# Kernel optimization log

Hardware: AMD Instinct MI355X
Metric: run time of the kernel (lower is better)

## Reference

```python
import jax, jax.numpy as jnp
import numpy as np

# Static config (matches init_kwargs)
THR = 0.2
BORDER = 2
TEMP = 0.1
H0C, W0C = 60, 80
H1C, W1C = 60, 80
HW0_I = (480, 640)
SCALE = HW0_I[0] / H0C  # = 8.0, coarse->image scale


def setup_inputs() -> dict:
    key = jax.random.key(0)
    k0, k1 = jax.random.split(key)
    feat0 = jax.random.normal(k0, (4, H0C * W0C, 256), dtype=jnp.float32)
    feat1 = jax.random.normal(k1, (4, H1C * W1C, 256), dtype=jnp.float32)
    return {"feat0": feat0, "feat1": feat1}


def _valid_axis(n):
    i = jnp.arange(n)
    return (i >= BORDER) & (i < n - BORDER)


def reference(feat0, feat1):
    B, L, C = feat0.shape
    S = feat1.shape[1]
    inv_sqrt_c = 1.0 / jnp.sqrt(jnp.asarray(C, feat0.dtype))
    f0 = feat0 * inv_sqrt_c
    f1 = feat1 * inv_sqrt_c
    # similarity + dual softmax -> confidence matrix [B, L, S]
    sim = jnp.einsum("blc,bsc->bls", f0, f1) / TEMP
    conf = jax.nn.softmax(sim, axis=1) * jax.nn.softmax(sim, axis=2)

    # threshold + border removal (static border, no padding masks)
    mask = conf > THR
    m5 = mask.reshape(B, H0C, W0C, H1C, W1C)
    m5 = (m5
          & _valid_axis(H0C)[None, :, None, None, None]
          & _valid_axis(W0C)[None, None, :, None, None]
          & _valid_axis(H1C)[None, None, None, :, None]
          & _valid_axis(W1C)[None, None, None, None, :])
    mask = m5.reshape(B, L, S)

    # mutual nearest: keep conf only where it is both the row max and the col max
    score = mask.astype(conf.dtype) * jnp.max(conf, axis=2, keepdims=True) * jnp.max(conf, axis=1, keepdims=True)
    mask_max_values = jnp.max(score, axis=2)          # [B, L]
    s_ids = jnp.argmax(score, axis=2)                 # [B, L]
    match = mask_max_values > 0                       # [B, L] dense stand-in for torch.where
    mconf = jnp.take_along_axis(conf, s_ids[:, :, None], axis=2)[..., 0]
    mconf = jnp.where(match, mconf, jnp.zeros_like(mconf))

    # coarse keypoint coordinates
    l = jnp.arange(L)
    mkpts0 = jnp.stack([l % W0C, l // W0C], axis=1).astype(conf.dtype) * SCALE          # [L, 2]
    mkpts1 = jnp.stack([s_ids % W1C, s_ids // W1C], axis=-1).astype(conf.dtype) * SCALE  # [B, L, 2]
    return conf, match, s_ids, mconf, mkpts0, mkpts1
```

## Files before the change

### kernel.cpp

```cpp
#include <hip/hip_runtime.h>
#include <math.h>

#define B_ 4
#define L_ 4800
#define S_ 4800
#define C_ 256
#define THR 0.2f
#define SIM_SCALE 0.0390625f
#define KPT_SCALE 8.0f

typedef short bf16x8 __attribute__((ext_vector_type(8)));
typedef float f32x4  __attribute__((ext_vector_type(4)));


__device__ __forceinline__ unsigned short f2bf(float x) {
    union { float f; unsigned int u; } v; v.f = x;
    unsigned int r = v.u + 0x7fffu + ((v.u >> 16) & 1u);
    return (unsigned short)(r >> 16);
}

__global__ void k_init(float* ws) {
    int i = blockIdx.x * blockDim.x + threadIdx.x;
    if (i < 76800) ws[i] = 0.0f;
}

__global__ void k_cast(const float* __restrict__ f0, const float* __restrict__ f1,
                       ushort* __restrict__ f0b, ushort* __restrict__ f1b) {
    int i = blockIdx.x * blockDim.x + threadIdx.x;
    if (i * 4 >= B_ * L_ * C_) return;
    float4 a = ((const float4*)f0)[i];
    float4 b = ((const float4*)f1)[i];
    ushort4 oa, ob;
    oa.x = f2bf(a.x); oa.y = f2bf(a.y); oa.z = f2bf(a.z); oa.w = f2bf(a.w);
    ob.x = f2bf(b.x); ob.y = f2bf(b.y); ob.z = f2bf(b.z); ob.w = f2bf(b.w);
    ((ushort4*)f0b)[i] = oa;
    ((ushort4*)f1b)[i] = ob;
}

__global__ __launch_bounds__(256) void k_gemm(
        const ushort* __restrict__ f0b, const ushort* __restrict__ f1b,
        float* __restrict__ p_out,
        float* __restrict__ rowsum, float* __restrict__ colsum) {
    const int b    = blockIdx.z;
    const int l0   = blockIdx.y * 64;
    const int wave = threadIdx.x >> 6;
    const int s0   = blockIdx.x * 256 + wave * 64;
    if (s0 >= S_) return;
    const int lane = threadIdx.x & 63;
    const int quad = lane >> 4;
    const int lr   = lane & 15;

    const ushort* A  = f0b + (size_t)b * L_ * C_;
    const ushort* Bm = f1b + (size_t)b * S_ * C_;

    f32x4 acc[4][4];
#pragma unroll
    for (int r = 0; r < 4; r++)
#pragma unroll
        for (int c = 0; c < 4; c++) acc[r][c] = (f32x4){0.f, 0.f, 0.f, 0.f};

    for (int kk = 0; kk < C_; kk += 32) {
        bf16x8 af[4], bf[4];
#pragma unroll
        for (int r = 0; r < 4; r++) {
            const int row = l0 + r * 16 + lr;
            af[r] = *(const bf16x8*)(A + (size_t)row * C_ + kk + quad * 8);
        }
#pragma unroll
        for (int c = 0; c < 4; c++) {
            const int srow = s0 + c * 16 + lr;
            bf[c] = *(const bf16x8*)(Bm + (size_t)srow * C_ + kk + quad * 8);
        }
#pragma unroll
        for (int r = 0; r < 4; r++)
#pragma unroll
            for (int c = 0; c < 4; c++)
                acc[r][c] = __builtin_amdgcn_mfma_f32_16x16x32_bf16(af[r], bf[c], acc[r][c], 0, 0, 0);
    }

#pragma unroll
    for (int r = 0; r < 4; r++)
#pragma unroll
        for (int c = 0; c < 4; c++)
#pragma unroll
            for (int g = 0; g < 4; g++)
                acc[r][c][g] = __expf(acc[r][c][g] * SIM_SCALE);

    float* pb = p_out + (size_t)b * L_ * S_;
#pragma unroll
    for (int r = 0; r < 4; r++)
#pragma unroll
        for (int g = 0; g < 4; g++) {
            const int row = l0 + r * 16 + quad * 4 + g;
            float* prow = pb + (size_t)row * S_ + s0 + lr;
#pragma unroll
            for (int c = 0; c < 4; c++) prow[c * 16] = acc[r][c][g];
        }

#pragma unroll
    for (int r = 0; r < 4; r++)
#pragma unroll
        for (int g = 0; g < 4; g++) {
            float v = acc[r][0][g] + acc[r][1][g] + acc[r][2][g] + acc[r][3][g];
            v += __shfl_xor(v, 1, 64);
            v += __shfl_xor(v, 2, 64);
            v += __shfl_xor(v, 4, 64);
            v += __shfl_xor(v, 8, 64);
            if (lr == 0) {
                const int row = l0 + r * 16 + quad * 4 + g;
                atomicAdd(rowsum + b * L_ + row, v);
            }
        }
#pragma unroll
    for (int c = 0; c < 4; c++) {
        float v = 0.f;
#pragma unroll
        for (int r = 0; r < 4; r++)
#pragma unroll
            for (int g = 0; g < 4; g++) v += acc[r][c][g];
        v += __shfl_xor(v, 16, 64);
        v += __shfl_xor(v, 32, 64);
        if (quad == 0) atomicAdd(colsum + b * S_ + s0 + c * 16 + lr, v);
    }
}

__global__ __launch_bounds__(256) void k_conf(
        float* __restrict__ conf,
        const float* __restrict__ rowsum, const float* __restrict__ colsum,
        float* __restrict__ rowmax, float* __restrict__ colmax) {
    const int b  = blockIdx.z;
    const int l0 = blockIdx.y * 64;
    const int s0 = blockIdx.x * 64;
    __shared__ unsigned rm[64], cm[64];
    const int t = threadIdx.x;
    if (t < 64) { rm[t] = 0u; cm[t] = 0u; }
    __syncthreads();
    const int c4 = t & 15, r0 = t >> 4;
    const float4 cs = *(const float4*)(colsum + b * S_ + s0 + c4 * 4);
    const float icx = 1.0f / cs.x, icy = 1.0f / cs.y, icz = 1.0f / cs.z, icw = 1.0f / cs.w;
    float cmx = 0.f, cmy = 0.f, cmz = 0.f, cmw = 0.f;
    float* base = conf + (size_t)b * L_ * S_;
#pragma unroll
    for (int it = 0; it < 4; it++) {
        const int r = r0 + 16 * it;
        const int l = l0 + r;
        const float irs = 1.0f / rowsum[b * L_ + l];
        float* addr = base + (size_t)l * S_ + s0 + c4 * 4;
        float4 p = *(float4*)addr;
        float4 cf;
        cf.x = p.x * p.x * (irs * icx);
        cf.y = p.y * p.y * (irs * icy);
        cf.z = p.z * p.z * (irs * icz);
        cf.w = p.w * p.w * (irs * icw);
        *(float4*)addr = cf;
        const float m = fmaxf(fmaxf(cf.x, cf.y), fmaxf(cf.z, cf.w));
        atomicMax(&rm[r], __float_as_uint(m));
        cmx = fmaxf(cmx, cf.x); cmy = fmaxf(cmy, cf.y);
        cmz = fmaxf(cmz, cf.z); cmw = fmaxf(cmw, cf.w);
    }
    atomicMax(&cm[c4 * 4 + 0], __float_as_uint(cmx));
    atomicMax(&cm[c4 * 4 + 1], __float_as_uint(cmy));
    atomicMax(&cm[c4 * 4 + 2], __float_as_uint(cmz));
    atomicMax(&cm[c4 * 4 + 3], __float_as_uint(cmw));
    __syncthreads();
    if (t < 64) {
        atomicMax((unsigned*)rowmax + b * L_ + l0 + t, rm[t]);
        atomicMax((unsigned*)colmax + b * S_ + s0 + t, cm[t]);
    }
}

__global__ __launch_bounds__(256) void k_match(
        const float* __restrict__ conf,
        const float* __restrict__ rowmax, const float* __restrict__ colmax,
        float* __restrict__ o_match, float* __restrict__ o_sids,
        float* __restrict__ o_mconf, float* __restrict__ o_kp0,
        float* __restrict__ o_kp1) {
    const int l = blockIdx.x;
    const int b = blockIdx.y;
    const int t = threadIdx.x;
    const int lh = l / 80, lw = l % 80;
    const bool lvalid = (lh >= 2 && lh < 58 && lw >= 2 && lw < 78);

    __shared__ float sv[256];
    __shared__ int   si[256];

    float bv = 0.0f; int bi = 0;
    if (lvalid) {
        const float* row = conf + ((size_t)b * L_ + l) * S_;
        const float  rmv = rowmax[b * L_ + l];
        const float* cmr = colmax + b * S_;
        for (int i = t; i < S_ / 4; i += 256) {
            const float4 cf = *(const float4*)(row + i * 4);
            float cv; int s;
#define PROC(comp, off)                                                        \
            cv = cf.comp; s = i * 4 + off;                                     \
            if (cv > THR) {                                                    \
                const int sh = s / 80, sw = s % 80;                            \
                if (sh >= 2 && sh < 58 && sw >= 2 && sw < 78) {                \
                    const float sc = rmv * cmr[s];                             \
                    if (sc > bv || (sc == bv && s < bi)) { bv = sc; bi = s; }  \
                }                                                              \
            }
            PROC(x, 0) PROC(y, 1) PROC(z, 2) PROC(w, 3)
#undef PROC
        }
    }
    sv[t] = bv; si[t] = bi;
    __syncthreads();
    for (int off = 128; off > 0; off >>= 1) {
        if (t < off) {
            const float v2 = sv[t + off]; const int i2 = si[t + off];
            if (v2 > sv[t] || (v2 == sv[t] && i2 < si[t])) { sv[t] = v2; si[t] = i2; }
        }
        __syncthreads();
    }
    if (t == 0) {
        const float maxv = sv[0]; const int sid = si[0];
        const bool match = maxv > 0.0f;
        float mc = 0.0f;
        if (match) mc = conf[((size_t)b * L_ + l) * S_ + sid];
        const int o = b * L_ + l;
        o_match[o] = match ? 1.0f : 0.0f;
        o_sids[o]  = (float)sid;
        o_mconf[o] = mc;
        o_kp1[o * 2 + 0] = (float)(sid % 80) * KPT_SCALE;
        o_kp1[o * 2 + 1] = (float)(sid / 80) * KPT_SCALE;
        if (b == 0) {
            o_kp0[l * 2 + 0] = (float)lw * KPT_SCALE;
            o_kp0[l * 2 + 1] = (float)lh * KPT_SCALE;
        }
    }
}

extern "C" void kernel_launch(void* const* d_in, const int* in_sizes, int n_in,
                              void* d_out, int out_size, void* d_ws, size_t ws_size,
                              hipStream_t stream) {
    const float* f0 = (const float*)d_in[0];
    const float* f1 = (const float*)d_in[1];
    float* out = (float*)d_out;

    float* conf_o  = out;
    float* o_match = out + (size_t)92160000;
    float* o_sids  = o_match + 19200;
    float* o_mconf = o_sids + 19200;
    float* o_kp0   = o_mconf + 19200;
    float* o_kp1   = o_kp0 + 9600;

    float* wsf    = (float*)d_ws;
    float* rowsum = wsf;
    float* colsum = wsf + 19200;
    float* rowmax = wsf + 38400;
    float* colmax = wsf + 57600;
    ushort* f0b = (ushort*)(wsf + 76800);
    ushort* f1b = f0b + (size_t)B_ * L_ * C_;

    k_init<<<300, 256, 0, stream>>>(wsf);
    k_cast<<<4800, 256, 0, stream>>>(f0, f1, f0b, f1b);
    k_gemm<<<dim3(19, 75, B_), 256, 0, stream>>>(f0b, f1b, conf_o, rowsum, colsum);
    k_conf<<<dim3(75, 75, B_), 256, 0, stream>>>(conf_o, rowsum, colsum, rowmax, colmax);
    k_match<<<dim3(L_, B_), 256, 0, stream>>>(conf_o, rowmax, colmax,
                                              o_match, o_sids, o_mconf, o_kp0, o_kp1);
}
```

Baseline: 754.7 us.

## Recompute GEMM in second pass to fuse normalization, maxima and sparse candidate extraction

Splits the similarity GEMM into two passes: the first only accumulates row/column sums of exp(sim), the second recomputes the tile, normalizes into conf, writes it once, updates row/col maxima, and appends above-threshold valid entries to a global candidate list. Separate scoring and emit kernels then resolve the per-row argmax via 64-bit atomicMax over candidates, replacing full-matrix read/rewrite and row-scan passes. This trades a second GEMM's compute for eliminating several passes over the large conf matrix, at the risk of overflowing the fixed candidate capacity.

Result: slower. 789.0 us (+4.5%).

```diff
diff --git a/kernel.cpp b/kernel.cpp
--- a/kernel.cpp
+++ b/kernel.cpp
@@ -8,10 +8,15 @@
 #define THR 0.2f
 #define SIM_SCALE 0.0390625f
 #define KPT_SCALE 8.0f
+#define CAND_CAP 262144u
 
 typedef short bf16x8 __attribute__((ext_vector_type(8)));
 typedef float f32x4  __attribute__((ext_vector_type(4)));
 
+#define WS_ZERO_N 115204
+#define WS_CAND_CNT 115200
+#define WS_CAND_LIST 115208
+#define WS_BF16 (115208 + CAND_CAP)
 
 __device__ __forceinline__ unsigned short f2bf(float x) {
     union { float f; unsigned int u; } v; v.f = x;
@@ -21,7 +26,7 @@
 
 __global__ void k_init(float* ws) {
     int i = blockIdx.x * blockDim.x + threadIdx.x;
-    if (i < 76800) ws[i] = 0.0f;
+    if (i < WS_ZERO_N) ws[i] = 0.0f;
 }
 
 __global__ void k_cast(const float* __restrict__ f0, const float* __restrict__ f1,
@@ -37,10 +42,13 @@
     ((ushort4*)f1b)[i] = ob;
 }
 
+template <int PASS>
 __global__ __launch_bounds__(256) void k_gemm(
         const ushort* __restrict__ f0b, const ushort* __restrict__ f1b,
-        float* __restrict__ p_out,
-        float* __restrict__ rowsum, float* __restrict__ colsum) {
+        float* __restrict__ conf,
+        float* __restrict__ rowsum, float* __restrict__ colsum,
+        float* __restrict__ rowmax, float* __restrict__ colmax,
+        unsigned* __restrict__ cand_cnt, unsigned* __restrict__ cand_list) {
     const int b    = blockIdx.z;
     const int l0   = blockIdx.y * 64;
     const int wave = threadIdx.x >> 6;
@@ -86,149 +94,161 @@
             for (int g = 0; g < 4; g++)
                 acc[r][c][g] = __expf(acc[r][c][g] * SIM_SCALE);
 
-    float* pb = p_out + (size_t)b * L_ * S_;
-#pragma unroll
-    for (int r = 0; r < 4; r++)
-#pragma unroll
-        for (int g = 0; g < 4; g++) {
-            const int row = l0 + r * 16 + quad * 4 + g;
-            float* prow = pb + (size_t)row * S_ + s0 + lr;
-#pragma unroll
-            for (int c = 0; c < 4; c++) prow[c * 16] = acc[r][c][g];
-        }
-
-#pragma unroll
-    for (int r = 0; r < 4; r++)
-#pragma unroll
-        for (int g = 0; g < 4; g++) {
-            float v = acc[r][0][g] + acc[r][1][g] + acc[r][2][g] + acc[r][3][g];
-            v += __shfl_xor(v, 1, 64);
-            v += __shfl_xor(v, 2, 64);
-            v += __shfl_xor(v, 4, 64);
-            v += __shfl_xor(v, 8, 64);
-            if (lr == 0) {
+    if constexpr (PASS == 0) {
+#pragma unroll
+        for (int r = 0; r < 4; r++)
+#pragma unroll
+            for (int g = 0; g < 4; g++) {
+                float v = acc[r][0][g] + acc[r][1][g] + acc[r][2][g] + acc[r][3][g];
+                v += __shfl_xor(v, 1, 64);
+                v += __shfl_xor(v, 2, 64);
+                v += __shfl_xor(v, 4, 64);
+                v += __shfl_xor(v, 8, 64);
+                if (lr == 0) {
+                    const int row = l0 + r * 16 + quad * 4 + g;
+                    atomicAdd(rowsum + b * L_ + row, v);
+                }
+            }
+#pragma unroll
+        for (int c = 0; c < 4; c++) {
+            float v = 0.f;
+#pragma unroll
+            for (int r = 0; r < 4; r++)
+#pragma unroll
+                for (int g = 0; g < 4; g++) v += acc[r][c][g];
+            v += __shfl_xor(v, 16, 64);
+            v += __shfl_xor(v, 32, 64);
+            if (quad == 0) atomicAdd(colsum + b * S_ + s0 + c * 16 + lr, v);
+        }
+    } else {
+        float irs[4][4];
+#pragma unroll
+        for (int r = 0; r < 4; r++)
+#pragma unroll
+            for (int g = 0; g < 4; g++)
+                irs[r][g] = 1.0f / rowsum[b * L_ + l0 + r * 16 + quad * 4 + g];
+        float ics[4];
+#pragma unroll
+        for (int c = 0; c < 4; c++)
+            ics[c] = 1.0f / colsum[b * S_ + s0 + c * 16 + lr];
+#pragma unroll
+        for (int r = 0; r < 4; r++)
+#pragma unroll
+            for (int c = 0; c < 4; c++)
+#pragma unroll
+                for (int g = 0; g < 4; g++) {
+                    const float p = acc[r][c][g];
+                    acc[r][c][g] = p * p * (irs[r][g] * ics[c]);
+                }
+
+        float* pb = conf + (size_t)b * L_ * S_;
+#pragma unroll
+        for (int r = 0; r < 4; r++)
+#pragma unroll
+            for (int g = 0; g < 4; g++) {
                 const int row = l0 + r * 16 + quad * 4 + g;
-                atomicAdd(rowsum + b * L_ + row, v);
+                float* prow = pb + (size_t)row * S_ + s0 + lr;
+#pragma unroll
+                for (int c = 0; c < 4; c++) prow[c * 16] = acc[r][c][g];
             }
-        }
-#pragma unroll
-    for (int c = 0; c < 4; c++) {
-        float v = 0.f;
-#pragma unroll
-        for (int r = 0; r < 4; r++)
-#pragma unroll
-            for (int g = 0; g < 4; g++) v += acc[r][c][g];
-        v += __shfl_xor(v, 16, 64);
-        v += __shfl_xor(v, 32, 64);
-        if (quad == 0) atomicAdd(colsum + b * S_ + s0 + c * 16 + lr, v);
-    }
-}
-
-__global__ __launch_bounds__(256) void k_conf(
-        float* __restrict__ conf,
-        const float* __restrict__ rowsum, const float* __restrict__ colsum,
-        float* __restrict__ rowmax, float* __restrict__ colmax) {
-    const int b  = blockIdx.z;
-    const int l0 = blockIdx.y * 64;
-    const int s0 = blockIdx.x * 64;
-    __shared__ unsigned rm[64], cm[64];
-    const int t = threadIdx.x;
-    if (t < 64) { rm[t] = 0u; cm[t] = 0u; }
-    __syncthreads();
-    const int c4 = t & 15, r0 = t >> 4;
-    const float4 cs = *(const float4*)(colsum + b * S_ + s0 + c4 * 4);
-    const float icx = 1.0f / cs.x, icy = 1.0f / cs.y, icz = 1.0f / cs.z, icw = 1.0f / cs.w;
-    float cmx = 0.f, cmy = 0.f, cmz = 0.f, cmw = 0.f;
-    float* base = conf + (size_t)b * L_ * S_;
-#pragma unroll
-    for (int it = 0; it < 4; it++) {
-        const int r = r0 + 16 * it;
-        const int l = l0 + r;
-        const float irs = 1.0f / rowsum[b * L_ + l];
-        float* addr = base + (size_t)l * S_ + s0 + c4 * 4;
-        float4 p = *(float4*)addr;
-        float4 cf;
-        cf.x = p.x * p.x * (irs * icx);
-        cf.y = p.y * p.y * (irs * icy);
-        cf.z = p.z * p.z * (irs * icz);
-        cf.w = p.w * p.w * (irs * icw);
-        *(float4*)addr = cf;
-        const float m = fmaxf(fmaxf(cf.x, cf.y), fmaxf(cf.z, cf.w));
-        atomicMax(&rm[r], __float_as_uint(m));
-        cmx = fmaxf(cmx, cf.x); cmy = fmaxf(cmy, cf.y);
-        cmz = fmaxf(cmz, cf.z); cmw = fmaxf(cmw, cf.w);
-    }
-    atomicMax(&cm[c4 * 4 + 0], __float_as_uint(cmx));
-    atomicMax(&cm[c4 * 4 + 1], __float_as_uint(cmy));
-    atomicMax(&cm[c4 * 4 + 2], __float_as_uint(cmz));
-    atomicMax(&cm[c4 * 4 + 3], __float_as_uint(cmw));
-    __syncthreads();
-    if (t < 64) {
-        atomicMax((unsigned*)rowmax + b * L_ + l0 + t, rm[t]);
-        atomicMax((unsigned*)colmax + b * S_ + s0 + t, cm[t]);
-    }
-}
-
-__global__ __launch_bounds__(256) void k_match(
-        const float* __restrict__ conf,
-        const float* __restrict__ rowmax, const float* __restrict__ colmax,
-        float* __restrict__ o_match, float* __restrict__ o_sids,
-        float* __restrict__ o_mconf, float* __restrict__ o_kp0,
-        float* __restrict__ o_kp1) {
-    const int l = blockIdx.x;
-    const int b = blockIdx.y;
-    const int t = threadIdx.x;
-    const int lh = l / 80, lw = l % 80;
-    const bool lvalid = (lh >= 2 && lh < 58 && lw >= 2 && lw < 78);
-
-    __shared__ float sv[256];
-    __shared__ int   si[256];
-
-    float bv = 0.0f; int bi = 0;
-    if (lvalid) {
-        const float* row = conf + ((size_t)b * L_ + l) * S_;
-        const float  rmv = rowmax[b * L_ + l];
-        const float* cmr = colmax + b * S_;
-        for (int i = t; i < S_ / 4; i += 256) {
-            const float4 cf = *(const float4*)(row + i * 4);
-            float cv; int s;
-#define PROC(comp, off)                                                        \
-            cv = cf.comp; s = i * 4 + off;                                     \
-            if (cv > THR) {                                                    \
-                const int sh = s / 80, sw = s % 80;                            \
-                if (sh >= 2 && sh < 58 && sw >= 2 && sw < 78) {                \
-                    const float sc = rmv * cmr[s];                             \
-                    if (sc > bv || (sc == bv && s < bi)) { bv = sc; bi = s; }  \
-                }                                                              \
+
+        float lane_max = 0.f;
+#pragma unroll
+        for (int r = 0; r < 4; r++)
+#pragma unroll
+            for (int g = 0; g < 4; g++) {
+                float m = fmaxf(fmaxf(acc[r][0][g], acc[r][1][g]),
+                                fmaxf(acc[r][2][g], acc[r][3][g]));
+                lane_max = fmaxf(lane_max, m);
+                m = fmaxf(m, __shfl_xor(m, 1, 64));
+                m = fmaxf(m, __shfl_xor(m, 2, 64));
+                m = fmaxf(m, __shfl_xor(m, 4, 64));
+                m = fmaxf(m, __shfl_xor(m, 8, 64));
+                if (lr == 0) {
+                    const int row = l0 + r * 16 + quad * 4 + g;
+                    atomicMax((unsigned*)rowmax + b * L_ + row, __float_as_uint(m));
+                }
             }
-            PROC(x, 0) PROC(y, 1) PROC(z, 2) PROC(w, 3)
-#undef PROC
-        }
-    }
-    sv[t] = bv; si[t] = bi;
-    __syncthreads();
-    for (int off = 128; off > 0; off >>= 1) {
-        if (t < off) {
-            const float v2 = sv[t + off]; const int i2 = si[t + off];
-            if (v2 > sv[t] || (v2 == sv[t] && i2 < si[t])) { sv[t] = v2; si[t] = i2; }
-        }
-        __syncthreads();
-    }
-    if (t == 0) {
-        const float maxv = sv[0]; const int sid = si[0];
-        const bool match = maxv > 0.0f;
-        float mc = 0.0f;
-        if (match) mc = conf[((size_t)b * L_ + l) * S_ + sid];
-        const int o = b * L_ + l;
-        o_match[o] = match ? 1.0f : 0.0f;
-        o_sids[o]  = (float)sid;
-        o_mconf[o] = mc;
-        o_kp1[o * 2 + 0] = (float)(sid % 80) * KPT_SCALE;
-        o_kp1[o * 2 + 1] = (float)(sid / 80) * KPT_SCALE;
-        if (b == 0) {
-            o_kp0[l * 2 + 0] = (float)lw * KPT_SCALE;
-            o_kp0[l * 2 + 1] = (float)lh * KPT_SCALE;
-        }
+#pragma unroll
+        for (int c = 0; c < 4; c++) {
+            float v = 0.f;
+#pragma unroll
+            for (int r = 0; r < 4; r++)
+#pragma unroll
+                for (int g = 0; g < 4; g++) v = fmaxf(v, acc[r][c][g]);
+            v = fmaxf(v, __shfl_xor(v, 16, 64));
+            v = fmaxf(v, __shfl_xor(v, 32, 64));
+            if (quad == 0)
+                atomicMax((unsigned*)colmax + b * S_ + s0 + c * 16 + lr, __float_as_uint(v));
+        }
+
+        if (__any(lane_max > THR)) {
+#pragma unroll
+            for (int r = 0; r < 4; r++)
+#pragma unroll
+                for (int c = 0; c < 4; c++)
+#pragma unroll
+                    for (int g = 0; g < 4; g++) {
+                        const float v = acc[r][c][g];
+                        if (v > THR) {
+                            const int l = l0 + r * 16 + quad * 4 + g;
+                            const int s = s0 + c * 16 + lr;
+                            const int lh = l / 80, lw = l % 80;
+                            const int sh = s / 80, sw = s % 80;
+                            if (lh >= 2 && lh < 58 && lw >= 2 && lw < 78 &&
+                                sh >= 2 && sh < 58 && sw >= 2 && sw < 78) {
+                                unsigned idx = atomicAdd(cand_cnt, 1u);
+                                if (idx < CAND_CAP)
+                                    cand_list[idx] = ((unsigned)b << 26) |
+                                                     ((unsigned)l << 13) | (unsigned)s;
+                            }
+                        }
+                    }
+        }
+    }
+}
+
+__global__ void k_score(const unsigned* __restrict__ cand_cnt,
+                        const unsigned* __restrict__ cand_list,
+                        const float* __restrict__ rowmax,
+                        const float* __restrict__ colmax,
+                        unsigned long long* __restrict__ best) {
+    const unsigned n = min(*cand_cnt, CAND_CAP);
+    for (unsigned i = blockIdx.x * blockDim.x + threadIdx.x; i < n;
+         i += gridDim.x * blockDim.x) {
+        const unsigned pk = cand_list[i];
+        const int b = pk >> 26;
+        const int l = (pk >> 13) & 8191;
+        const int s = pk & 8191;
+        const float sc = rowmax[b * L_ + l] * colmax[b * S_ + s];
+        const unsigned long long key =
+            ((unsigned long long)__float_as_uint(sc) << 32) |
+            (unsigned long long)(0xFFFFFFFFu - (unsigned)s);
+        atomicMax(best + b * L_ + l, key);
+    }
+}
+
+__global__ void k_emit(const float* __restrict__ conf,
+                       const unsigned long long* __restrict__ best,
+                       float* __restrict__ o_match, float* __restrict__ o_sids,
+                       float* __restrict__ o_mconf, float* __restrict__ o_kp0,
+                       float* __restrict__ o_kp1) {
+    const int i = blockIdx.x * blockDim.x + threadIdx.x;
+    if (i >= B_ * L_) return;
+    const int b = i / L_;
+    const int l = i - b * L_;
+    const unsigned long long key = best[i];
+    const bool match = key != 0ull;
+    const int sid = match ? (int)(0xFFFFFFFFu - (unsigned)(key & 0xFFFFFFFFull)) : 0;
+    const float mc = match ? conf[(size_t)i * S_ + sid] : 0.0f;
+    o_match[i] = match ? 1.0f : 0.0f;
+    o_sids[i]  = (float)sid;
+    o_mconf[i] = mc;
+    o_kp1[i * 2 + 0] = (float)(sid % 80) * KPT_SCALE;
+    o_kp1[i * 2 + 1] = (float)(sid / 80) * KPT_SCALE;
+    if (b == 0) {
+        o_kp0[l * 2 + 0] = (float)(l % 80) * KPT_SCALE;
+        o_kp0[l * 2 + 1] = (float)(l / 80) * KPT_SCALE;
     }
 }
 
@@ -251,13 +271,18 @@
     float* colsum = wsf + 19200;
     float* rowmax = wsf + 38400;
     float* colmax = wsf + 57600;
-    ushort* f0b = (ushort*)(wsf + 76800);
+    unsigned long long* best = (unsigned long long*)(wsf + 76800);
+    unsigned* cand_cnt  = (unsigned*)(wsf + WS_CAND_CNT);
+    unsigned* cand_list = (unsigned*)(wsf + WS_CAND_LIST);
+    ushort* f0b = (ushort*)(wsf + WS_BF16);
     ushort* f1b = f0b + (size_t)B_ * L_ * C_;
 
-    k_init<<<300, 256, 0, stream>>>(wsf);
+    k_init<<<(WS_ZERO_N + 255) / 256, 256, 0, stream>>>(wsf);
     k_cast<<<4800, 256, 0, stream>>>(f0, f1, f0b, f1b);
-    k_gemm<<<dim3(19, 75, B_), 256, 0, stream>>>(f0b, f1b, conf_o, rowsum, colsum);
-    k_conf<<<dim3(75, 75, B_), 256, 0, stream>>>(conf_o, rowsum, colsum, rowmax, colmax);
-    k_match<<<dim3(L_, B_), 256, 0, stream>>>(conf_o, rowmax, colmax,
-                                              o_match, o_sids, o_mconf, o_kp0, o_kp1);
-}
+    k_gemm<0><<<dim3(19, 75, B_), 256, 0, stream>>>(
+        f0b, f1b, conf_o, rowsum, colsum, rowmax, colmax, cand_cnt, cand_list);
+    k_gemm<1><<<dim3(19, 75, B_), 256, 0, stream>>>(
+        f0b, f1b, conf_o, rowsum, colsum, rowmax, colmax, cand_cnt, cand_list);
+    k_score<<<64, 256, 0, stream>>>(cand_cnt, cand_list, rowmax, colmax, best);
+    k_emit<<<75, 256, 0, stream>>>(conf_o, best, o_match, o_sids, o_mconf, o_kp0, o_kp1);
+}
```
